# Performance work log

Measured on AMD Instinct MI355X. Metric: run time of the kernel, lower is better.

The kernel has to match this reference:

```python
import jax, jax.numpy as jnp
import numpy as np

B, N, M, D, H = 8, 4096, 1024, 1024, 16
HD = D // H  # head_dim = 64
SCALE = HD ** -0.5
EPS = 1e-6


def _ln(x, g, b):
    mu = jnp.mean(x, axis=-1, keepdims=True)
    var = jnp.mean((x - mu) ** 2, axis=-1, keepdims=True)
    return (x - mu) * jax.lax.rsqrt(var + EPS) * g + b


def setup_inputs() -> dict:
    key = jax.random.key(0)
    ks = jax.random.split(key, 10)
    s = 0.02
    return {
        "x": jax.random.normal(ks[0], (B, N, D), jnp.float32),
        "wavelet_tokens": jax.random.normal(ks[1], (B, M, D), jnp.float32),
        "ln_q_g": jnp.ones((D,), jnp.float32),
        "ln_q_b": jnp.zeros((D,), jnp.float32),
        "Wq": jax.random.normal(ks[2], (D, D), jnp.float32) * s,
        "bq": jnp.zeros((D,), jnp.float32),
        "ln_kv_g": jnp.ones((D,), jnp.float32),
        "ln_kv_b": jnp.zeros((D,), jnp.float32),
        "Wkv": jax.random.normal(ks[3], (D, 2 * D), jnp.float32) * s,
        "bkv": jnp.zeros((2 * D,), jnp.float32),
        "Wo": jax.random.normal(ks[4], (D, D), jnp.float32) * s,
        "bo": jnp.zeros((D,), jnp.float32),
        "ln_f_g": jnp.ones((D,), jnp.float32),
        "ln_f_b": jnp.zeros((D,), jnp.float32),
        "W1": jax.random.normal(ks[5], (D, 4 * D), jnp.float32) * s,
        "b1": jnp.zeros((4 * D,), jnp.float32),
        "W2": jax.random.normal(ks[6], (4 * D, D), jnp.float32) * s,
        "b2": jnp.zeros((D,), jnp.float32),
    }


def reference(x, wavelet_tokens, ln_q_g, ln_q_b, Wq, bq, ln_kv_g, ln_kv_b,
              Wkv, bkv, Wo, bo, ln_f_g, ln_f_b, W1, b1, W2, b2):
    residual = x
    q = _ln(x, ln_q_g, ln_q_b) @ Wq + bq            # [B,N,D]
    kv = _ln(wavelet_tokens, ln_kv_g, ln_kv_b) @ Wkv + bkv  # [B,M,2D]
    k, v = kv[..., :D], kv[..., D:]
    q = q.reshape(B, N, H, HD).transpose(0, 2, 1, 3)  # [B,H,N,d]
    k = k.reshape(B, M, H, HD).transpose(0, 2, 1, 3)  # [B,H,M,d]
    v = v.reshape(B, M, H, HD).transpose(0, 2, 1, 3)
    q = jax.nn.softmax(q, axis=2) * SCALE   # softmax over spatial N
    k = jax.nn.softmax(k, axis=-1)          # softmax over head_dim
    context = jnp.einsum('bhmd,bhme->bhde', k, v)   # [B,H,d,d]
    out = jnp.einsum('bhnd,bhde->bhne', q, context)  # [B,H,N,d]
    out = out.transpose(0, 2, 1, 3).reshape(B, N, D)
    out = out @ Wo + bo
    x2 = residual + out
    h = _ln(x2, ln_f_g, ln_f_b) @ W1 + b1
    h = jax.nn.silu(h) @ W2 + b2
    return x2 + h
```

## Files before the change

kernel.cpp:

```cpp
#include <hip/hip_runtime.h>
#include <stdint.h>
#include <stddef.h>

#define BB 8
#define NN 4096
#define MTOK 1024
#define DD 1024
#define HH 16
#define EPSF 1e-6f
static const float SCALE_F = 0.125f;

typedef __attribute__((ext_vector_type(4))) float f32x4;
typedef __attribute__((ext_vector_type(8))) short bf16x8;

__device__ __forceinline__ short f2bf(float f) {
  union { float f; uint32_t u; } x; x.f = f;
  uint32_t r = (x.u + 0x7fffu + ((x.u >> 16) & 1u)) >> 16;
  return (short)(uint16_t)r;
}
__device__ __forceinline__ float bf2f(short s) {
  union { uint32_t u; float f; } x; x.u = ((uint32_t)(uint16_t)s) << 16;
  return x.f;
}

#if defined(__HIP_DEVICE_COMPILE__) && __has_builtin(__builtin_amdgcn_global_load_lds)
#define USE_GLOAD_LDS 1
#else
#define USE_GLOAD_LDS 0
#endif

#define BAR() __builtin_amdgcn_s_barrier()
#define LGKM0()                                        \
  do {                                                 \
    asm volatile("s_waitcnt lgkmcnt(0)" ::: "memory"); \
    __builtin_amdgcn_sched_barrier(0);                 \
  } while (0)
#define LGKM8() asm volatile("s_waitcnt lgkmcnt(8)" ::: "memory")
#if USE_GLOAD_LDS
#define VMW6() asm volatile("s_waitcnt vmcnt(6)" ::: "memory")
#else
#define VMW6() asm volatile("s_waitcnt vmcnt(0) lgkmcnt(0)" ::: "memory")
#endif
#define VMW0() asm volatile("s_waitcnt vmcnt(0)" ::: "memory")

__device__ __forceinline__ bf16x8 ldsld(const char* p, int off) {
  return *(const bf16x8*)(p + off);
}
template <int MH>
__device__ __forceinline__ void rdA8(const char* k0, const char* k1, bf16x8 a[4][2]) {
#pragma unroll
  for (int m = 0; m < 4; ++m) {
    a[m][0] = ldsld(k0, MH * 8192 + m * 2048);
    a[m][1] = ldsld(k1, MH * 8192 + m * 2048);
  }
}
template <int NH>
__device__ __forceinline__ void rdB4(const char* k0, const char* k1, bf16x8 b[2][2]) {
#pragma unroll
  for (int n = 0; n < 2; ++n) {
    b[n][0] = ldsld(k0, NH * 16384 + n * 2048);
    b[n][1] = ldsld(k1, NH * 16384 + n * 2048);
  }
}
__device__ __forceinline__ void stgA(char* smc, int base, const short* pg,
                                     int ld, int mh, int k, int w) {
#pragma unroll
  for (int i = 0; i < 2; ++i) {
    const short* src = pg + (long)(mh * 64 + i * 128) * ld + k;
    char* dst = smc + base + i * 16384 + mh * 8192 + w * 1024;
#if USE_GLOAD_LDS
    __builtin_amdgcn_global_load_lds(
        (const __attribute__((address_space(1))) void*)src,
        (__attribute__((address_space(3))) void*)dst, 16, 0, 0);
#else
    *(bf16x8*)(dst + (int)(threadIdx.x & 63) * 16) = *(const bf16x8*)src;
#endif
  }
}
__device__ __forceinline__ void stgB(char* smc, int base, const short* pg,
                                     int ld, int h, int k, int w) {
#pragma unroll
  for (int i = 0; i < 2; ++i) {
    const short* src = pg + (long)(h * 32 + i * 128) * ld + k;
    char* dst = smc + base + h * 16384 + i * 8192 + w * 1024;
#if USE_GLOAD_LDS
    __builtin_amdgcn_global_load_lds(
        (const __attribute__((address_space(1))) void*)src,
        (__attribute__((address_space(3))) void*)dst, 16, 0, 0);
#else
    *(bf16x8*)(dst + (int)(threadIdx.x & 63) * 16) = *(const bf16x8*)src;
#endif
  }
}
template <int MH, int NH>
__device__ __forceinline__ void mq(const bf16x8 a[4][2], const bf16x8 b[2][2],
                                   f32x4 acc[8][4]) {
  __builtin_amdgcn_s_setprio(1);
#pragma unroll
  for (int m = 0; m < 4; ++m)
#pragma unroll
    for (int n = 0; n < 2; ++n) {
      f32x4 c = acc[MH * 4 + m][NH * 2 + n];
      c = __builtin_amdgcn_mfma_f32_16x16x32_bf16(a[m][0], b[n][0], c, 0, 0, 0);
      c = __builtin_amdgcn_mfma_f32_16x16x32_bf16(a[m][1], b[n][1], c, 0, 0, 0);
      acc[MH * 4 + m][NH * 2 + n] = c;
    }
  __builtin_amdgcn_s_setprio(0);
}

template <int EPI>
__global__ __launch_bounds__(512, 2) void gemm256(
    const short* __restrict__ A, const short* __restrict__ BT,
    const float* __restrict__ bias, const float* __restrict__ resid,
    void* __restrict__ outp, int N, int K, int lda, int ldb, int num_n) {
  __shared__ int4 smem4[131072 / 16];
  char* smc = (char*)smem4;
  const int t = threadIdx.x;
  const int w = t >> 6, lane = t & 63;
  const int wr = w >> 2, wc = w & 3;

  const int nwg = gridDim.x, orig = blockIdx.x;
  const int q8 = nwg >> 3, r8 = nwg & 7;
  const int xcd = orig & 7, loc = orig >> 3;
  const int wg = (xcd < r8 ? xcd * (q8 + 1) : r8 * (q8 + 1) + (xcd - r8) * q8) + loc;
  const int bm = wg / num_n, bn = wg % num_n;

  const int T = K >> 6;

  int LA = wr * 16384 + (lane & 15) * 128 + ((lane >> 4) << 4);
  LA ^= ((LA >> 7) & 7) << 4;
  int LB = wc * 4096 + (lane & 15) * 128 + ((lane >> 4) << 4);
  LB ^= ((LB >> 7) & 7) << 4;
  const char* pA0k0 = smc + LA;
  const char* pA0k1 = smc + (LA ^ 64);
  const char* pA1k0 = pA0k0 + 65536;
  const char* pA1k1 = pA0k1 + 65536;
  const char* pB0k0 = smc + 32768 + LB;
  const char* pB0k1 = smc + 32768 + (LB ^ 64);
  const char* pB1k0 = pB0k0 + 65536;
  const char* pB1k1 = pB0k1 + 65536;

  const int colswz = ((t & 7) ^ ((t >> 3) & 7)) * 8;
  const short* pAg = A + (long)(bm * 256 + (t >> 3)) * lda + colswz;
  const short* pBg =
      BT + (long)(bn * 256 + ((t >> 8) * 64 + ((t >> 3) & 31))) * ldb + colswz;

  f32x4 acc[8][4];
#pragma unroll
  for (int i = 0; i < 8; ++i)
#pragma unroll
    for (int j = 0; j < 4; ++j) acc[i][j] = (f32x4){0.f, 0.f, 0.f, 0.f};

  bf16x8 a[4][2], b0[2][2], b1[2][2];

  stgA(smc, 0, pAg, lda, 0, 0, w);
  stgB(smc, 32768, pBg, ldb, 0, 0, w);
  stgB(smc, 32768, pBg, ldb, 1, 0, w);
  stgA(smc, 0, pAg, lda, 1, 0, w);
  stgA(smc, 65536, pAg, lda, 0, 64, w);
  stgB(smc, 98304, pBg, ldb, 0, 64, w);
  stgB(smc, 98304, pBg, ldb, 1, 64, w);
  VMW6();
  BAR();

  for (int t2 = 0; t2 < T; t2 += 2) {
    const int k1 = (t2 + 1) * 64;
    const int k2 = (t2 + 2 < T ? t2 + 2 : 0) * 64;
    const int k3 = (t2 + 3 < T ? t2 + 3 : 0) * 64;
    rdA8<0>(pA0k0, pA0k1, a);
    rdB4<0>(pB0k0, pB0k1, b0);
    stgA(smc, 65536, pAg, lda, 1, k1, w);
    LGKM8();
    BAR(); LGKM0();
    mq<0, 0>(a, b0, acc);
    BAR();
    rdB4<1>(pB0k0, pB0k1, b1);
    stgA(smc, 0, pAg, lda, 0, k2, w);
    BAR(); LGKM0();
    mq<0, 1>(a, b1, acc);
    BAR();
    rdA8<1>(pA0k0, pA0k1, a);
    stgB(smc, 32768, pBg, ldb, 0, k2, w);
    BAR(); LGKM0();
    mq<1, 0>(a, b0, acc);
    BAR();
    stgB(smc, 32768, pBg, ldb, 1, k2, w);
    VMW6();
    BAR();
    mq<1, 1>(a, b1, acc);
    BAR();
    rdA8<0>(pA1k0, pA1k1, a);
    rdB4<0>(pB1k0, pB1k1, b0);
    stgA(smc, 0, pAg, lda, 1, k2, w);
    LGKM8();
    BAR(); LGKM0();
    mq<0, 0>(a, b0, acc);
    BAR();
    rdB4<1>(pB1k0, pB1k1, b1);
    stgA(smc, 65536, pAg, lda, 0, k3, w);
    BAR(); LGKM0();
    mq<0, 1>(a, b1, acc);
    BAR();
    rdA8<1>(pA1k0, pA1k1, a);
    stgB(smc, 98304, pBg, ldb, 0, k3, w);
    BAR(); LGKM0();
    mq<1, 0>(a, b0, acc);
    BAR();
    stgB(smc, 98304, pBg, ldb, 1, k3, w);
    VMW6();
    BAR();
    mq<1, 1>(a, b1, acc);
    BAR();
  }
  VMW0();

  const int r0 = bm * 256 + wr * 128 + ((lane >> 4) << 2);
  const int c0 = bn * 256 + wc * 64 + (lane & 15);
#pragma unroll
  for (int mi = 0; mi < 8; ++mi) {
#pragma unroll
    for (int ni = 0; ni < 4; ++ni) {
      const int col = c0 + ni * 16;
      const float bv = bias ? bias[col] : 0.f;
#pragma unroll
      for (int rr = 0; rr < 4; ++rr) {
        const int row = r0 + mi * 16 + rr;
        const long idx = (long)row * N + col;
        float v = acc[mi][ni][rr] + bv;
        if (EPI == 0) {
          ((float*)outp)[idx] = v;
        } else if (EPI == 1) {
          ((float*)outp)[idx] = v + resid[idx];
        } else if (EPI == 2) {
          ((short*)outp)[idx] = f2bf(v);
        } else {
          v = v / (1.f + __expf(-v));
          ((short*)outp)[idx] = f2bf(v);
        }
      }
    }
  }
}

__global__ __launch_bounds__(256) void ln_rows(const float* __restrict__ in,
                                               const float* __restrict__ g,
                                               const float* __restrict__ bta,
                                               short* __restrict__ outp) {
  const int row = blockIdx.x;
  const int t = threadIdx.x;
  const float4 v = ((const float4*)(in + (long)row * DD))[t];
  float s = v.x + v.y + v.z + v.w;
  float ss = v.x * v.x + v.y * v.y + v.z * v.z + v.w * v.w;
#pragma unroll
  for (int off = 1; off < 64; off <<= 1) {
    s += __shfl_xor(s, off);
    ss += __shfl_xor(ss, off);
  }
  __shared__ float red[8];
  const int w = t >> 6, lane = t & 63;
  if (lane == 0) { red[w] = s; red[4 + w] = ss; }
  __syncthreads();
  s = red[0] + red[1] + red[2] + red[3];
  ss = red[4] + red[5] + red[6] + red[7];
  const float mu = s * (1.f / DD);
  const float var = ss * (1.f / DD) - mu * mu;
  const float rs = rsqrtf(var + EPSF);
  const float4 gv = ((const float4*)g)[t];
  const float4 bv = ((const float4*)bta)[t];
  short4 o;
  o.x = f2bf((v.x - mu) * rs * gv.x + bv.x);
  o.y = f2bf((v.y - mu) * rs * gv.y + bv.y);
  o.z = f2bf((v.z - mu) * rs * gv.z + bv.z);
  o.w = f2bf((v.w - mu) * rs * gv.w + bv.w);
  ((short4*)(outp + (long)row * DD))[t] = o;
}

__global__ __launch_bounds__(256) void tconv(const float* __restrict__ W,
                                             short* __restrict__ WT, int K, int N) {
  __shared__ float tile[64][65];
  const int k0 = blockIdx.x * 64, n0 = blockIdx.y * 64;
  const int t = threadIdx.x;
  const int tr = t >> 6, tc = t & 63;
#pragma unroll
  for (int i = 0; i < 64; i += 4)
    tile[i + tr][tc] = W[(long)(k0 + i + tr) * N + n0 + tc];
  __syncthreads();
#pragma unroll
  for (int i = 0; i < 64; i += 4)
    WT[(long)(n0 + i + tr) * K + k0 + tc] = f2bf(tile[tc][i + tr]);
}

__global__ __launch_bounds__(256) void ctx_kernel(const short* __restrict__ kv,
                                                  float* __restrict__ ctx) {
  const int bh = blockIdx.x;
  const int b = bh >> 4, h = bh & 15;
  const int t = threadIdx.x, g = t >> 6, lane = t & 63;
  __shared__ float ksm[4][64];
  __shared__ float vsm[4][64];
  float acc[16];
#pragma unroll
  for (int j = 0; j < 16; ++j) acc[j] = 0.f;
  const int d = t & 63;
  const int e0 = (t >> 6) * 16;
  const short* base = kv + (long)b * MTOK * 2048 + h * 64;
  for (int m0 = 0; m0 < MTOK; m0 += 4) {
    const long moff = (long)(m0 + g) * 2048;
    float kval = bf2f(base[moff + lane]);
    float vval = bf2f(base[moff + 1024 + lane]);
    float mx = kval;
#pragma unroll
    for (int off = 1; off < 64; off <<= 1) mx = fmaxf(mx, __shfl_xor(mx, off));
    float e = __expf(kval - mx);
    float sm = e;
#pragma unroll
    for (int off = 1; off < 64; off <<= 1) sm += __shfl_xor(sm, off);
    ksm[g][lane] = e / sm;
    vsm[g][lane] = vval;
    __syncthreads();
#pragma unroll
    for (int mm = 0; mm < 4; ++mm) {
      const float kd = ksm[mm][d];
#pragma unroll
      for (int j = 0; j < 16; ++j) acc[j] = fmaf(kd, vsm[mm][e0 + j], acc[j]);
    }
    __syncthreads();
  }
  float* cp = ctx + ((long)bh * 64 + d) * 64 + e0;
#pragma unroll
  for (int j = 0; j < 16; ++j) cp[j] = acc[j];
}

__global__ __launch_bounds__(256) void qstat_part(const short* __restrict__ q,
                                                  float* __restrict__ pmax,
                                                  float* __restrict__ psum) {
  const int c = blockIdx.x * 256 + threadIdx.x;
  const int b = blockIdx.z, ch = blockIdx.y;
  const short* qp = q + ((long)b * NN + ch * 128) * DD + c;
  float mx = -1e30f, sm = 0.f;
  for (int r = 0; r < 128; ++r) {
    const float xv = bf2f(qp[(long)r * DD]);
    const float nm = fmaxf(mx, xv);
    sm = sm * __expf(mx - nm) + __expf(xv - nm);
    mx = nm;
  }
  const long idx = ((long)b * DD + c) * 32 + ch;
  pmax[idx] = mx;
  psum[idx] = sm;
}

__global__ __launch_bounds__(256) void qstat_comb(const float* __restrict__ pmax,
                                                  const float* __restrict__ psum,
                                                  float* __restrict__ cmax,
                                                  float* __restrict__ crs) {
  const int i = blockIdx.x * 256 + threadIdx.x;
  const float* pm = pmax + (long)i * 32;
  const float* ps = psum + (long)i * 32;
  float mx = -1e30f;
#pragma unroll
  for (int ch = 0; ch < 32; ++ch) mx = fmaxf(mx, pm[ch]);
  float sm = 0.f;
#pragma unroll
  for (int ch = 0; ch < 32; ++ch) sm += ps[ch] * __expf(pm[ch] - mx);
  cmax[i] = mx;
  crs[i] = SCALE_F / sm;
}

__global__ __launch_bounds__(256) void attn_apply(const short* __restrict__ q,
                                                  const float* __restrict__ ctx,
                                                  const float* __restrict__ cmax,
                                                  const float* __restrict__ crs,
                                                  short* __restrict__ outa) {
  const int b = blockIdx.z, h = blockIdx.y, n0 = blockIdx.x * 128;
  const int t = threadIdx.x, g = t >> 6, lane = t & 63;
  __shared__ float ctx_l[4096];
  __shared__ float cm[64], cs[64];
  __shared__ float qsm[4][64];
  const float* cp = ctx + (long)(b * HH + h) * 4096;
  for (int i = t; i < 4096; i += 256) ctx_l[i] = cp[i];
  if (t < 64) {
    cm[t] = cmax[(long)b * DD + h * 64 + t];
    cs[t] = crs[(long)b * DD + h * 64 + t];
  }
  __syncthreads();
  for (int i = 0; i < 32; ++i) {
    const int n = n0 + i * 4 + g;
    const long off = ((long)b * NN + n) * DD + h * 64;
    const float qv = bf2f(q[off + lane]);
    const float qs = __expf(qv - cm[lane]) * cs[lane];
    qsm[g][lane] = qs;
    float o = 0.f;
#pragma unroll
    for (int dd = 0; dd < 64; ++dd) o = fmaf(qsm[g][dd], ctx_l[dd * 64 + lane], o);
    outa[off + lane] = f2bf(o);
  }
}

extern "C" void kernel_launch(void* const* d_in, const int* in_sizes, int n_in,
                              void* d_out, int out_size, void* d_ws, size_t ws_size,
                              hipStream_t stream) {
  (void)in_sizes; (void)n_in; (void)out_size;
  const float* x      = (const float*)d_in[0];
  const float* wav    = (const float*)d_in[1];
  const float* ln_q_g = (const float*)d_in[2];
  const float* ln_q_b = (const float*)d_in[3];
  const float* Wq     = (const float*)d_in[4];
  const float* bq     = (const float*)d_in[5];
  const float* ln_kv_g= (const float*)d_in[6];
  const float* ln_kv_b= (const float*)d_in[7];
  const float* Wkv    = (const float*)d_in[8];
  const float* bkv    = (const float*)d_in[9];
  const float* Wo     = (const float*)d_in[10];
  const float* bo     = (const float*)d_in[11];
  const float* ln_f_g = (const float*)d_in[12];
  const float* ln_f_b = (const float*)d_in[13];
  const float* W1     = (const float*)d_in[14];
  const float* b1     = (const float*)d_in[15];
  const float* W2     = (const float*)d_in[16];
  const float* b2     = (const float*)d_in[17];
  float* outp = (float*)d_out;
  char* ws = (char*)d_ws;

  const long MR = (long)BB * NN;
  const long MKV = (long)BB * MTOK;

  size_t off = 0;
  auto bump = [&](size_t bytes) {
    size_t o = off;
    off += (bytes + 255) & ~(size_t)255;
    return o;
  };
  short* WqT  = (short*)(ws + bump((size_t)DD * DD * 2));
  short* WkvT = (short*)(ws + bump((size_t)2048 * DD * 2));
  short* WoT  = (short*)(ws + bump((size_t)DD * DD * 2));
  short* W1T  = (short*)(ws + bump((size_t)4096 * DD * 2));
  short* W2T  = (short*)(ws + bump((size_t)DD * 4096 * 2));
  float* qbuf = (float*)(ws + bump((size_t)MR * DD * 4));
  short* lnbuf= (short*)(ws + bump((size_t)MR * DD * 2));
  float* ctx  = (float*)(ws + bump((size_t)BB * HH * 64 * 64 * 4));
  float* pmax = (float*)(ws + bump((size_t)BB * DD * 32 * 4));
  float* psum = (float*)(ws + bump((size_t)BB * DD * 32 * 4));
  float* cmax = (float*)(ws + bump((size_t)BB * DD * 4));
  float* crs  = (float*)(ws + bump((size_t)BB * DD * 4));
  const size_t dyn0 = off;
  short* wvln  = (short*)(ws + dyn0);
  short* kvbuf = (short*)(ws + dyn0 + (size_t)MKV * DD * 2);
  short* oattn = (short*)(ws + dyn0);
  short* hbuf  = (short*)(ws + dyn0);

  size_t avail = ws_size > dyn0 ? ws_size - dyn0 : 0;
  int CS = 4096;
  while (CS > 256 && (size_t)MR * CS * 2 > avail) CS >>= 1;

  const int nm = (int)(MR / 256);
  const int nmkv = (int)(MKV / 256);

  tconv<<<dim3(DD / 64, DD / 64), 256, 0, stream>>>(Wq, WqT, DD, DD);
  tconv<<<dim3(DD / 64, 2048 / 64), 256, 0, stream>>>(Wkv, WkvT, DD, 2048);
  tconv<<<dim3(DD / 64, DD / 64), 256, 0, stream>>>(Wo, WoT, DD, DD);
  tconv<<<dim3(DD / 64, 4096 / 64), 256, 0, stream>>>(W1, W1T, DD, 4096);
  tconv<<<dim3(4096 / 64, DD / 64), 256, 0, stream>>>(W2, W2T, 4096, DD);

  ln_rows<<<dim3((unsigned)MR), 256, 0, stream>>>(x, ln_q_g, ln_q_b, lnbuf);
  ln_rows<<<dim3((unsigned)MKV), 256, 0, stream>>>(wav, ln_kv_g, ln_kv_b, wvln);

  gemm256<2><<<dim3((unsigned)(nm * (DD / 256))), 512, 0, stream>>>(
      lnbuf, WqT, bq, nullptr, (short*)qbuf, DD, DD, DD, DD, DD / 256);
  gemm256<2><<<dim3((unsigned)(nmkv * (2048 / 256))), 512, 0, stream>>>(
      wvln, WkvT, bkv, nullptr, kvbuf, 2048, DD, DD, DD, 2048 / 256);
  ctx_kernel<<<dim3(BB * HH), 256, 0, stream>>>(kvbuf, ctx);
  qstat_part<<<dim3(DD / 256, 32, BB), 256, 0, stream>>>((const short*)qbuf, pmax, psum);
  qstat_comb<<<dim3(BB * DD / 256), 256, 0, stream>>>(pmax, psum, cmax, crs);
  attn_apply<<<dim3(NN / 128, HH, BB), 256, 0, stream>>>((const short*)qbuf, ctx,
                                                         cmax, crs, oattn);
  gemm256<1><<<dim3((unsigned)(nm * (DD / 256))), 512, 0, stream>>>(
      oattn, WoT, bo, x, qbuf, DD, DD, DD, DD, DD / 256);
  float* x2 = qbuf;
  ln_rows<<<dim3((unsigned)MR), 256, 0, stream>>>(x2, ln_f_g, ln_f_b, lnbuf);
  for (int c0 = 0; c0 < 4096; c0 += CS) {
    gemm256<3><<<dim3((unsigned)(nm * (CS / 256))), 512, 0, stream>>>(
        lnbuf, W1T + (long)c0 * DD, b1 + c0, nullptr, hbuf, CS, DD, DD, DD, CS / 256);
    gemm256<1><<<dim3((unsigned)(nm * (DD / 256))), 512, 0, stream>>>(
        hbuf, W2T + c0, (c0 == 0) ? b2 : nullptr,
        (c0 == 0) ? (const float*)x2 : (const float*)outp, outp, DD, CS, CS, 4096, DD / 256);
  }
}
```

Before: 1.285 ms.

## Double-buffer LDS fragment registers to overlap reads with MFMA in GEMM loop

```diff
diff --git a/kernel.cpp b/kernel.cpp
--- a/kernel.cpp
+++ b/kernel.cpp
@@ -29,17 +29,20 @@
 #define USE_GLOAD_LDS 0
 #endif
 
-#define BAR() __builtin_amdgcn_s_barrier()
+#define BAR() asm volatile("s_barrier" ::: "memory")
 #define LGKM0()                                        \
   do {                                                 \
     asm volatile("s_waitcnt lgkmcnt(0)" ::: "memory"); \
     __builtin_amdgcn_sched_barrier(0);                 \
   } while (0)
-#define LGKM8() asm volatile("s_waitcnt lgkmcnt(8)" ::: "memory")
 #if USE_GLOAD_LDS
-#define VMW6() asm volatile("s_waitcnt vmcnt(6)" ::: "memory")
+#define VMW8() asm volatile("s_waitcnt vmcnt(8)" ::: "memory")
+#define VMW10() asm volatile("s_waitcnt vmcnt(10)" ::: "memory")
+#define LGKM4() asm volatile("s_waitcnt lgkmcnt(4)" ::: "memory")
 #else
-#define VMW6() asm volatile("s_waitcnt vmcnt(0) lgkmcnt(0)" ::: "memory")
+#define VMW8() asm volatile("s_waitcnt vmcnt(0) lgkmcnt(0)" ::: "memory")
+#define VMW10() asm volatile("s_waitcnt vmcnt(0) lgkmcnt(0)" ::: "memory")
+#define LGKM4() asm volatile("s_waitcnt lgkmcnt(0)" ::: "memory")
 #endif
 #define VMW0() asm volatile("s_waitcnt vmcnt(0)" ::: "memory")
 
@@ -151,65 +154,67 @@
 #pragma unroll
     for (int j = 0; j < 4; ++j) acc[i][j] = (f32x4){0.f, 0.f, 0.f, 0.f};
 
-  bf16x8 a[4][2], b0[2][2], b1[2][2];
+  bf16x8 A0[4][2], A1[4][2], Bn0[2][2], Bn1[2][2];
 
   stgA(smc, 0, pAg, lda, 0, 0, w);
   stgB(smc, 32768, pBg, ldb, 0, 0, w);
   stgB(smc, 32768, pBg, ldb, 1, 0, w);
   stgA(smc, 0, pAg, lda, 1, 0, w);
   stgA(smc, 65536, pAg, lda, 0, 64, w);
+  stgB(smc, 98304, pBg, ldb, 1, 64, w);
   stgB(smc, 98304, pBg, ldb, 0, 64, w);
-  stgB(smc, 98304, pBg, ldb, 1, 64, w);
-  VMW6();
+  stgA(smc, 65536, pAg, lda, 1, 64, w);
+  VMW8();
   BAR();
+  rdA8<0>(pA0k0, pA0k1, A0);
+  rdB4<0>(pB0k0, pB0k1, Bn0);
+  LGKM0();
+  BAR();
 
   for (int t2 = 0; t2 < T; t2 += 2) {
-    const int k1 = (t2 + 1) * 64;
     const int k2 = (t2 + 2 < T ? t2 + 2 : 0) * 64;
     const int k3 = (t2 + 3 < T ? t2 + 3 : 0) * 64;
-    rdA8<0>(pA0k0, pA0k1, a);
-    rdB4<0>(pB0k0, pB0k1, b0);
-    stgA(smc, 65536, pAg, lda, 1, k1, w);
-    LGKM8();
-    BAR(); LGKM0();
-    mq<0, 0>(a, b0, acc);
-    BAR();
-    rdB4<1>(pB0k0, pB0k1, b1);
+    VMW10();
+    rdB4<1>(pB0k0, pB0k1, Bn1);
     stgA(smc, 0, pAg, lda, 0, k2, w);
-    BAR(); LGKM0();
-    mq<0, 1>(a, b1, acc);
-    BAR();
-    rdA8<1>(pA0k0, pA0k1, a);
+    mq<0, 0>(A0, Bn0, acc);
+    BAR();
+    VMW10();
+    rdA8<1>(pA0k0, pA0k1, A1);
     stgB(smc, 32768, pBg, ldb, 0, k2, w);
-    BAR(); LGKM0();
-    mq<1, 0>(a, b0, acc);
-    BAR();
+    mq<0, 1>(A0, Bn1, acc);
+    BAR();
+    VMW10();
+    rdA8<0>(pA1k0, pA1k1, A0);
     stgB(smc, 32768, pBg, ldb, 1, k2, w);
-    VMW6();
-    BAR();
-    mq<1, 1>(a, b1, acc);
-    BAR();
-    rdA8<0>(pA1k0, pA1k1, a);
-    rdB4<0>(pB1k0, pB1k1, b0);
+    mq<1, 1>(A1, Bn1, acc);
+    BAR();
+    VMW10();
+    rdB4<1>(pB1k0, pB1k1, Bn1);
     stgA(smc, 0, pAg, lda, 1, k2, w);
-    LGKM8();
-    BAR(); LGKM0();
-    mq<0, 0>(a, b0, acc);
-    BAR();
-    rdB4<1>(pB1k0, pB1k1, b1);
+    LGKM4();
+    mq<1, 0>(A1, Bn0, acc);
+    BAR();
+    VMW10();
+    rdB4<0>(pB1k0, pB1k1, Bn0);
     stgA(smc, 65536, pAg, lda, 0, k3, w);
-    BAR(); LGKM0();
-    mq<0, 1>(a, b1, acc);
-    BAR();
-    rdA8<1>(pA1k0, pA1k1, a);
+    mq<0, 1>(A0, Bn1, acc);
+    BAR();
+    VMW10();
+    rdA8<1>(pA1k0, pA1k1, A1);
+    stgB(smc, 98304, pBg, ldb, 1, k3, w);
+    mq<0, 0>(A0, Bn0, acc);
+    BAR();
+    VMW10();
+    rdA8<0>(pA0k0, pA0k1, A0);
     stgB(smc, 98304, pBg, ldb, 0, k3, w);
-    BAR(); LGKM0();
-    mq<1, 0>(a, b0, acc);
-    BAR();
-    stgB(smc, 98304, pBg, ldb, 1, k3, w);
-    VMW6();
-    BAR();
-    mq<1, 1>(a, b1, acc);
+    mq<1, 0>(A1, Bn0, acc);
+    BAR();
+    VMW10();
+    rdB4<0>(pB0k0, pB0k1, Bn0);
+    stgA(smc, 65536, pAg, lda, 1, k3, w);
+    LGKM4();
+    mq<1, 1>(A1, Bn1, acc);
     BAR();
   }
   VMW0();
```

Measured after the change: 1.381 ms. 1.07x slower.
